# Kernel optimization log

Hardware: AMD Instinct MI355X
Metric: run time of the kernel (lower is better)

Reference implementation:

```python
import jax, jax.numpy as jnp
import numpy as np


def setup_inputs() -> dict:
    key = jax.random.key(0)
    ks = jax.random.split(key, 20)
    B, T, E, U, D, O = 64, 2048, 256, 256, 256, 32000
    s = lambda k, shp, fan: (jax.random.normal(k, shp, jnp.float32) * (1.0 / np.sqrt(fan)))
    return {
        'inputs': jax.random.normal(ks[0], (B, D), jnp.float32),
        'stm': jax.random.normal(ks[1], (B, U), jnp.float32),
        'x_seq': jax.random.normal(ks[2], (B, T, E), jnp.float32),
        'V_a': s(ks[3], (U + E,), U + E),
        'W_a': s(ks[4], (U + E, U + E), U + E),
        'W_r': s(ks[5], (D, U), D), 'U_r': s(ks[6], (U, U), U), 'C_r': s(ks[7], (E, U), E), 'b_r': jnp.zeros((U,), jnp.float32),
        'W_z': s(ks[8], (D, U), D), 'U_z': s(ks[9], (U, U), U), 'C_z': s(ks[10], (E, U), E), 'b_z': jnp.zeros((U,), jnp.float32),
        'W_p': s(ks[11], (D, U), D), 'U_p': s(ks[12], (U, U), U), 'C_p': s(ks[13], (E, U), E), 'b_p': jnp.zeros((U,), jnp.float32),
        'W_o': s(ks[14], (D, O), D), 'U_o': s(ks[15], (U, O), U), 'C_o': s(ks[16], (E, O), E), 'b_o': jnp.zeros((O,), jnp.float32),
    }


def reference(inputs, stm, x_seq, V_a, W_a,
              W_r, U_r, C_r, b_r,
              W_z, U_z, C_z, b_z,
              W_p, U_p, C_p, b_p,
              W_o, U_o, C_o, b_o):
    B, T, E = x_seq.shape
    U = stm.shape[-1]
    # Bahdanau additive attention: concat repeated state with encoder seq
    _stm = jnp.broadcast_to(stm[:, None, :], (B, T, U))          # [B,T,U]
    cat = jnp.concatenate([_stm, x_seq], axis=-1)                 # [B,T,U+E]
    et = jnp.einsum('btc,c->bt', jnp.tanh(jnp.einsum('btc,cd->btd', cat, W_a)), V_a)
    at = jax.nn.softmax(et, axis=1)                               # exp / sum over T
    context = jnp.einsum('bt,bte->be', at, x_seq)                 # [B,E]
    # GRU-style gates conditioned on input, previous state, and context
    rt = jax.nn.sigmoid(inputs @ W_r + stm @ U_r + context @ C_r + b_r)
    zt = jax.nn.sigmoid(inputs @ W_z + stm @ U_z + context @ C_z + b_z)
    s_tp = jnp.tanh(inputs @ W_p + (rt * stm) @ U_p + context @ C_p + b_p)
    st = (1.0 - zt) * stm + zt * s_tp                             # new state [B,U]
    output = jax.nn.softmax(inputs @ W_o + stm @ U_o + context @ C_o + b_o, axis=-1)  # [B,O]
    return output, st
```

## Files before the change

### kernel.cpp

```cpp
#include <hip/hip_runtime.h>
#include <hip/hip_bf16.h>

#define B_ 64
#define T_ 2048
#define E_ 256
#define U_ 256
#define O_ 32000
#define UE_ 512

typedef __attribute__((ext_vector_type(8))) short bf16x8;
typedef __attribute__((ext_vector_type(4))) float f32x4;

__device__ __forceinline__ unsigned short f2bf(float f){
  __hip_bfloat16 h = __float2bfloat16(f);
  return __builtin_bit_cast(unsigned short, h);
}
__device__ __forceinline__ unsigned pk2bf(float a, float b){
  return (unsigned)f2bf(a) | ((unsigned)f2bf(b) << 16);
}
__device__ __forceinline__ bf16x8 pack8(const float* v0, const float* v1){
  float4 x = *(const float4*)v0;
  float4 y = *(const float4*)v1;
  uint4 pk;
  pk.x = pk2bf(x.x, x.y); pk.y = pk2bf(x.z, x.w);
  pk.z = pk2bf(y.x, y.y); pk.w = pk2bf(y.z, y.w);
  return __builtin_bit_cast(bf16x8, pk);
}
__device__ __forceinline__ float ftanh(float x){
  float e = __expf(2.0f*x);
  return 1.0f - 2.0f/(e + 1.0f);
}
__device__ __forceinline__ float fsig(float x){
  return 1.0f/(1.0f + __expf(-x));
}

__global__ void pack_b_kernel(const float* __restrict__ Wa, unsigned short* __restrict__ bpack){
  int idx = blockIdx.x*256 + threadIdx.x;
  int n = idx & 511;
  int ktg = idx >> 9;
  int erow = ktg * 8;
  unsigned short o[8];
#pragma unroll
  for (int i = 0; i < 8; ++i)
    o[i] = f2bf(Wa[(256 + erow + i)*512 + n]);
  uint4 v;
  v.x = (unsigned)o[0] | ((unsigned)o[1] << 16);
  v.y = (unsigned)o[2] | ((unsigned)o[3] << 16);
  v.z = (unsigned)o[4] | ((unsigned)o[5] << 16);
  v.w = (unsigned)o[6] | ((unsigned)o[7] << 16);
  ((uint4*)bpack)[idx] = v;
}

__global__ __launch_bounds__(256)
void stmpart_mfma_kernel(const float* __restrict__ stm, const float* __restrict__ Wa,
                         float* __restrict__ sp){
  int tid = threadIdx.x;
  int w = tid >> 6, l = tid & 63, c = l & 15, g = l >> 4;
  int n0 = blockIdx.x*64 + w*16;
  f32x4 zero = {0.f,0.f,0.f,0.f};
  f32x4 acc[4];
#pragma unroll
  for (int mt = 0; mt < 4; ++mt) acc[mt] = zero;
#pragma unroll
  for (int ks = 0; ks < 8; ++ks){
    int kg = ks*32 + 8*g;
    bf16x8 a[4];
#pragma unroll
    for (int mt = 0; mt < 4; ++mt){
      const float* ap = stm + (mt*16 + c)*256 + kg;
      a[mt] = pack8(ap, ap + 4);
    }
    const float* bpt = Wa + (size_t)kg*512 + n0 + c;
    float bv[8];
#pragma unroll
    for (int i = 0; i < 8; ++i) bv[i] = bpt[(size_t)i*512];
    uint4 pk;
    pk.x = pk2bf(bv[0], bv[1]); pk.y = pk2bf(bv[2], bv[3]);
    pk.z = pk2bf(bv[4], bv[5]); pk.w = pk2bf(bv[6], bv[7]);
    bf16x8 bfr = __builtin_bit_cast(bf16x8, pk);
#pragma unroll
    for (int mt = 0; mt < 4; ++mt)
      acc[mt] = __builtin_amdgcn_mfma_f32_16x16x32_bf16(a[mt], bfr, acc[mt], 0, 0, 0);
  }
#pragma unroll
  for (int mt = 0; mt < 4; ++mt)
#pragma unroll
    for (int r = 0; r < 4; ++r){
      int m = mt*16 + 4*g + r;
      sp[m*512 + n0 + c] = acc[mt][r];
    }
}

__global__ __launch_bounds__(512, 4)
void et_kernel(const float* __restrict__ xseq, const unsigned short* __restrict__ bpack,
               const float* __restrict__ va, const float* __restrict__ sp,
               float* __restrict__ et){
  __shared__ __align__(16) uint4 sA4[2048];
  __shared__ float sVa[512];
  __shared__ float sSp[512];
  __shared__ float sEt[8][64];
  int tid = threadIdx.x;
  int m0 = blockIdx.x * 64;
  int b  = m0 >> 11;

  const float4* x4 = (const float4*)xseq + (size_t)m0 * 64;
  uint2* sA2 = (uint2*)sA4;
#pragma unroll
  for (int i = 0; i < 8; ++i){
    int p = i*512 + tid;
    int row = p >> 6, kq = p & 63;
    float4 v = x4[row*64 + kq];
    uint2 u;
    u.x = pk2bf(v.x, v.y);
    u.y = pk2bf(v.z, v.w);
    int s = ((row>>4)*8 + (kq>>3))*64 + ((kq>>1)&3)*16 + (row&15);
    sA2[(s ^ ((s>>4)&7))*2 + (kq&1)] = u;
  }
  sVa[tid < 512 ? tid : 0] = va[tid];
  sSp[tid] = sp[b*512 + tid];
  __syncthreads();

  int w = tid >> 6, l = tid & 63, c = l & 15, g = l >> 4;
  f32x4 zero = {0.f, 0.f, 0.f, 0.f};
  f32x4 acc[4][4];
#pragma unroll
  for (int mt = 0; mt < 4; ++mt)
#pragma unroll
    for (int nt = 0; nt < 4; ++nt) acc[mt][nt] = zero;

  const bf16x8* bp = (const bf16x8*)bpack;
#pragma unroll
  for (int ks = 0; ks < 8; ++ks){
    bf16x8 a[4], bb[4];
#pragma unroll
    for (int mt = 0; mt < 4; ++mt){
      int idx = (mt*8 + ks)*64 + l;
      a[mt] = *(const bf16x8*)&sA4[idx ^ ((idx>>4)&7)];
    }
    int bbase = (ks*4 + g)*512 + w*64 + c;
#pragma unroll
    for (int nt = 0; nt < 4; ++nt)
      bb[nt] = bp[bbase + nt*16];
#pragma unroll
    for (int mt = 0; mt < 4; ++mt)
#pragma unroll
      for (int nt = 0; nt < 4; ++nt)
        acc[mt][nt] = __builtin_amdgcn_mfma_f32_16x16x32_bf16(a[mt], bb[nt], acc[mt][nt], 0, 0, 0);
  }

  float pr[4][4];
#pragma unroll
  for (int mt = 0; mt < 4; ++mt)
#pragma unroll
    for (int r = 0; r < 4; ++r){
      float p = 0.f;
#pragma unroll
      for (int nt = 0; nt < 4; ++nt){
        int n = w*64 + nt*16 + c;
        float v = acc[mt][nt][r] + sSp[n];
        p += sVa[n] * ftanh(v);
      }
      pr[mt][r] = p;
    }
#pragma unroll
  for (int mask = 1; mask < 16; mask <<= 1){
#pragma unroll
    for (int mt = 0; mt < 4; ++mt)
#pragma unroll
      for (int r = 0; r < 4; ++r)
        pr[mt][r] += __shfl_xor(pr[mt][r], mask, 64);
  }
  if (c == 0){
#pragma unroll
    for (int mt = 0; mt < 4; ++mt)
#pragma unroll
      for (int r = 0; r < 4; ++r)
        sEt[w][mt*16 + 4*g + r] = pr[mt][r];
  }
  __syncthreads();
  if (tid < 64){
    float e = 0.f;
#pragma unroll
    for (int ww = 0; ww < 8; ++ww) e += sEt[ww][tid];
    et[m0 + tid] = e;
  }
}

__global__ void at_kernel(const float* __restrict__ et, float* __restrict__ at){
  __shared__ float red[4];
  __shared__ float red2[4];
  int b = blockIdx.x, tid = threadIdx.x;
  float v[8];
#pragma unroll
  for (int i = 0; i < 8; ++i) v[i] = et[b*2048 + i*256 + tid];
  float m = v[0];
#pragma unroll
  for (int i = 1; i < 8; ++i) m = fmaxf(m, v[i]);
#pragma unroll
  for (int off = 1; off < 64; off <<= 1) m = fmaxf(m, __shfl_xor(m, off, 64));
  int wv = tid >> 6;
  if ((tid & 63) == 0) red[wv] = m;
  __syncthreads();
  m = fmaxf(fmaxf(red[0], red[1]), fmaxf(red[2], red[3]));
  float e[8]; float s = 0.f;
#pragma unroll
  for (int i = 0; i < 8; ++i){ e[i] = __expf(v[i] - m); s += e[i]; }
#pragma unroll
  for (int off = 1; off < 64; off <<= 1) s += __shfl_xor(s, off, 64);
  if ((tid & 63) == 0) red2[wv] = s;
  __syncthreads();
  s = red2[0] + red2[1] + red2[2] + red2[3];
  float inv = 1.0f / s;
#pragma unroll
  for (int i = 0; i < 8; ++i) at[b*2048 + i*256 + tid] = e[i] * inv;
}

__global__ void ctxpart_kernel(const float* __restrict__ at, const float* __restrict__ xseq,
                               float* __restrict__ cp){
  __shared__ float s_at[256];
  int ch = blockIdx.x;
  int b  = blockIdx.y;
  int e  = threadIdx.x;
  int t0 = ch * 256;
  s_at[e] = at[b*2048 + t0 + e];
  __syncthreads();
  float acc = 0.f;
  const float* xp = xseq + ((size_t)(b*2048 + t0))*256 + e;
#pragma unroll 4
  for (int tt = 0; tt < 256; ++tt)
    acc += s_at[tt] * xp[(size_t)tt * 256];
  cp[(b*8 + ch)*256 + e] = acc;
}

__global__ void ctx_x1_kernel(const float* __restrict__ cp, const float* __restrict__ inputs,
                              const float* __restrict__ stm,
                              unsigned short* __restrict__ X1bf){
  int b = blockIdx.x, e = threadIdx.x;
  float s = 0.f;
#pragma unroll
  for (int c = 0; c < 8; ++c) s += cp[(b*8 + c)*256 + e];
  X1bf[b*768 + e]        = f2bf(inputs[b*256 + e]);
  X1bf[b*768 + 256 + e]  = f2bf(stm[b*256 + e]);
  X1bf[b*768 + 512 + e]  = f2bf(s);
}

__global__ __launch_bounds__(256)
void gates1_kernel(const unsigned short* __restrict__ X1bf, const float* __restrict__ stm,
                   const float* __restrict__ Wr, const float* __restrict__ Ur,
                   const float* __restrict__ Cr, const float* __restrict__ brr,
                   const float* __restrict__ Wz, const float* __restrict__ Uz,
                   const float* __restrict__ Cz, const float* __restrict__ bzz,
                   const float* __restrict__ Wp, const float* __restrict__ Cp,
                   const float* __restrict__ bpp,
                   float* __restrict__ rs, float* __restrict__ ztb, float* __restrict__ pic){
  int tid = threadIdx.x;
  int w = tid >> 6, l = tid & 63, c = l & 15, g = l >> 4;
  int n0 = blockIdx.x*64 + w*16;
  int gate = n0 >> 8;
  int col0 = n0 & 255;
  const float* W0; const float* W1; const float* W2; const float* bias;
  if (gate == 0){ W0 = Wr; W1 = Ur; W2 = Cr; bias = brr; }
  else if (gate == 1){ W0 = Wz; W1 = Uz; W2 = Cz; bias = bzz; }
  else { W0 = Wp; W1 = nullptr; W2 = Cp; bias = bpp; }

  f32x4 zero = {0.f,0.f,0.f,0.f};
  f32x4 acc[4];
#pragma unroll
  for (int mt = 0; mt < 4; ++mt) acc[mt] = zero;

#pragma unroll
  for (int ph = 0; ph < 3; ++ph){
    const float* src = (ph == 0) ? W0 : (ph == 1) ? W1 : W2;
    if (src == nullptr) continue;
#pragma unroll
    for (int ks = 0; ks < 8; ++ks){
      int kg = ks*32 + 8*g;
      bf16x8 a[4];
#pragma unroll
      for (int mt = 0; mt < 4; ++mt)
        a[mt] = *(const bf16x8*)&X1bf[(mt*16 + c)*768 + ph*256 + kg];
      const float* bpt = src + (size_t)kg*256 + col0 + c;
      float bv[8];
#pragma unroll
      for (int i = 0; i < 8; ++i) bv[i] = bpt[(size_t)i*256];
      uint4 pk;
      pk.x = pk2bf(bv[0], bv[1]); pk.y = pk2bf(bv[2], bv[3]);
      pk.z = pk2bf(bv[4], bv[5]); pk.w = pk2bf(bv[6], bv[7]);
      bf16x8 bfr = __builtin_bit_cast(bf16x8, pk);
#pragma unroll
      for (int mt = 0; mt < 4; ++mt)
        acc[mt] = __builtin_amdgcn_mfma_f32_16x16x32_bf16(a[mt], bfr, acc[mt], 0, 0, 0);
    }
  }

  int n = col0 + c;
  float bi = bias[n];
#pragma unroll
  for (int mt = 0; mt < 4; ++mt)
#pragma unroll
    for (int r = 0; r < 4; ++r){
      int m = mt*16 + 4*g + r;
      float pre = acc[mt][r] + bi;
      if (gate == 0)      rs[m*256 + n]  = fsig(pre) * stm[m*256 + n];
      else if (gate == 1) ztb[m*256 + n] = fsig(pre);
      else                pic[m*256 + n] = pre;
    }
}

__global__ __launch_bounds__(256)
void gates2_kernel(const float* __restrict__ rs, const float* __restrict__ Up,
                   const float* __restrict__ pic, const float* __restrict__ ztb,
                   const float* __restrict__ stm, float* __restrict__ stout){
  int tid = threadIdx.x;
  int w = tid >> 6, l = tid & 63, c = l & 15, g = l >> 4;
  int n0 = blockIdx.x*64 + w*16;
  f32x4 zero = {0.f,0.f,0.f,0.f};
  f32x4 acc[4];
#pragma unroll
  for (int mt = 0; mt < 4; ++mt) acc[mt] = zero;
#pragma unroll
  for (int ks = 0; ks < 8; ++ks){
    int kg = ks*32 + 8*g;
    bf16x8 a[4];
#pragma unroll
    for (int mt = 0; mt < 4; ++mt){
      const float* ap = rs + (mt*16 + c)*256 + kg;
      a[mt] = pack8(ap, ap + 4);
    }
    const float* bpt = Up + (size_t)kg*256 + n0 + c;
    float bv[8];
#pragma unroll
    for (int i = 0; i < 8; ++i) bv[i] = bpt[(size_t)i*256];
    uint4 pk;
    pk.x = pk2bf(bv[0], bv[1]); pk.y = pk2bf(bv[2], bv[3]);
    pk.z = pk2bf(bv[4], bv[5]); pk.w = pk2bf(bv[6], bv[7]);
    bf16x8 bfr = __builtin_bit_cast(bf16x8, pk);
#pragma unroll
    for (int mt = 0; mt < 4; ++mt)
      acc[mt] = __builtin_amdgcn_mfma_f32_16x16x32_bf16(a[mt], bfr, acc[mt], 0, 0, 0);
  }
#pragma unroll
  for (int mt = 0; mt < 4; ++mt)
#pragma unroll
    for (int r = 0; r < 4; ++r){
      int m = mt*16 + 4*g + r;
      int o = m*256 + n0 + c;
      float ap = pic[o] + acc[mt][r];
      float z = ztb[o];
      stout[o] = (1.f - z)*stm[o] + z*ftanh(ap);
    }
}

__global__ __launch_bounds__(256)
void logits_mfma_kernel(const unsigned short* __restrict__ X1bf,
                        const float* __restrict__ Wo, const float* __restrict__ Uo,
                        const float* __restrict__ Co, const float* __restrict__ boo,
                        float* __restrict__ outl){
  int tid = threadIdx.x;
  int w = tid >> 6, l = tid & 63, c = l & 15, g = l >> 4;
  int n0 = blockIdx.x*64 + w*16;
  f32x4 zero = {0.f,0.f,0.f,0.f};
  f32x4 acc[4];
#pragma unroll
  for (int mt = 0; mt < 4; ++mt) acc[mt] = zero;

#pragma unroll
  for (int ph = 0; ph < 3; ++ph){
    const float* src = (ph == 0) ? Wo : (ph == 1) ? Uo : Co;
#pragma unroll 2
    for (int ks = 0; ks < 8; ++ks){
      int kg = ph*256 + ks*32 + 8*g;
      bf16x8 a[4];
#pragma unroll
      for (int mt = 0; mt < 4; ++mt)
        a[mt] = *(const bf16x8*)&X1bf[(mt*16 + c)*768 + kg];
      const float* bpt = src + (size_t)(ks*32 + 8*g)*32000 + n0 + c;
      float bv[8];
#pragma unroll
      for (int i = 0; i < 8; ++i) bv[i] = bpt[(size_t)i*32000];
      uint4 pk;
      pk.x = pk2bf(bv[0], bv[1]);
      pk.y = pk2bf(bv[2], bv[3]);
      pk.z = pk2bf(bv[4], bv[5]);
      pk.w = pk2bf(bv[6], bv[7]);
      bf16x8 bfr = __builtin_bit_cast(bf16x8, pk);
#pragma unroll
      for (int mt = 0; mt < 4; ++mt)
        acc[mt] = __builtin_amdgcn_mfma_f32_16x16x32_bf16(a[mt], bfr, acc[mt], 0, 0, 0);
    }
  }

  float bias = boo[n0 + c];
#pragma unroll
  for (int mt = 0; mt < 4; ++mt)
#pragma unroll
    for (int r = 0; r < 4; ++r){
      int m = mt*16 + 4*g + r;
      outl[(size_t)m*32000 + n0 + c] = acc[mt][r] + bias;
    }
}

__global__ void sm_part_kernel(const float* __restrict__ logits, float* __restrict__ part){
  __shared__ float red[4];
  __shared__ float red2[4];
  int bid = blockIdx.x;
  int b = bid >> 3, ch = bid & 7;
  int base = b*32000 + ch*4000;
  int tid = threadIdx.x;
  float v[16];
#pragma unroll
  for (int i = 0; i < 16; ++i){
    int idx = i*256 + tid;
    v[i] = (idx < 4000) ? logits[base + idx] : -INFINITY;
  }
  float m = v[0];
#pragma unroll
  for (int i = 1; i < 16; ++i) m = fmaxf(m, v[i]);
#pragma unroll
  for (int off = 1; off < 64; off <<= 1) m = fmaxf(m, __shfl_xor(m, off, 64));
  int wv = tid >> 6;
  if ((tid & 63) == 0) red[wv] = m;
  __syncthreads();
  m = fmaxf(fmaxf(red[0], red[1]), fmaxf(red[2], red[3]));
  float s = 0.f;
#pragma unroll
  for (int i = 0; i < 16; ++i) s += __expf(v[i] - m);
#pragma unroll
  for (int off = 1; off < 64; off <<= 1) s += __shfl_xor(s, off, 64);
  if ((tid & 63) == 0) red2[wv] = s;
  __syncthreads();
  if (tid == 0){
    float st = red2[0] + red2[1] + red2[2] + red2[3];
    part[bid*2]     = m;
    part[bid*2 + 1] = st;
  }
}

__global__ void sm_norm_kernel(float* __restrict__ logits, const float* __restrict__ part){
  int bid = blockIdx.x;
  int b = bid >> 3, ch = bid & 7;
  int base = b*32000 + ch*4000;
  int tid = threadIdx.x;
  float M = -INFINITY;
#pragma unroll
  for (int cc = 0; cc < 8; ++cc) M = fmaxf(M, part[(b*8 + cc)*2]);
  float S = 0.f;
#pragma unroll
  for (int cc = 0; cc < 8; ++cc) S += part[(b*8 + cc)*2 + 1] * __expf(part[(b*8 + cc)*2] - M);
  float inv = 1.0f / S;
#pragma unroll
  for (int i = 0; i < 16; ++i){
    int idx = i*256 + tid;
    if (idx < 4000){
      int o = base + idx;
      logits[o] = __expf(logits[o] - M) * inv;
    }
  }
}

extern "C" void kernel_launch(void* const* d_in, const int* in_sizes, int n_in,
                              void* d_out, int out_size, void* d_ws, size_t ws_size,
                              hipStream_t stream) {
  const float* inputs = (const float*)d_in[0];
  const float* stm    = (const float*)d_in[1];
  const float* xseq   = (const float*)d_in[2];
  const float* Va     = (const float*)d_in[3];
  const float* Wa     = (const float*)d_in[4];
  const float* Wr = (const float*)d_in[5];
  const float* Ur = (const float*)d_in[6];
  const float* Cr = (const float*)d_in[7];
  const float* br = (const float*)d_in[8];
  const float* Wz = (const float*)d_in[9];
  const float* Uz = (const float*)d_in[10];
  const float* Cz = (const float*)d_in[11];
  const float* bz = (const float*)d_in[12];
  const float* Wp = (const float*)d_in[13];
  const float* Up = (const float*)d_in[14];
  const float* Cp = (const float*)d_in[15];
  const float* bp = (const float*)d_in[16];
  const float* Wo = (const float*)d_in[17];
  const float* Uo = (const float*)d_in[18];
  const float* Co = (const float*)d_in[19];
  const float* bo = (const float*)d_in[20];

  float* out   = (float*)d_out;
  float* stout = out + (size_t)B_*O_;

  float* wsf = (float*)d_ws;
  unsigned short* bpack = (unsigned short*)d_ws;
  float* sp   = wsf + 65536;
  float* et   = wsf + 98304;
  float* at   = wsf + 229376;
  float* cp   = wsf + 360448;
  unsigned short* X1bf = (unsigned short*)(wsf + 491520);
  float* part = wsf + 516096;
  float* rs   = wsf + 517120;
  float* ztb  = wsf + 533504;
  float* pic  = wsf + 549888;

  pack_b_kernel<<<64, 256, 0, stream>>>(Wa, bpack);
  stmpart_mfma_kernel<<<8, 256, 0, stream>>>(stm, Wa, sp);
  et_kernel<<<2048, 512, 0, stream>>>(xseq, bpack, Va, sp, et);
  at_kernel<<<64, 256, 0, stream>>>(et, at);
  ctxpart_kernel<<<dim3(8, 64), 256, 0, stream>>>(at, xseq, cp);
  ctx_x1_kernel<<<64, 256, 0, stream>>>(cp, inputs, stm, X1bf);
  gates1_kernel<<<12, 256, 0, stream>>>(X1bf, stm, Wr, Ur, Cr, br,
                                        Wz, Uz, Cz, bz, Wp, Cp, bp,
                                        rs, ztb, pic);
  gates2_kernel<<<4, 256, 0, stream>>>(rs, Up, pic, ztb, stm, stout);
  logits_mfma_kernel<<<500, 256, 0, stream>>>(X1bf, Wo, Uo, Co, bo, out);
  sm_part_kernel<<<512, 256, 0, stream>>>(out, part);
  sm_norm_kernel<<<512, 256, 0, stream>>>(out, part);
}
```

Measured before the change: 175.2 us.

## Fuse softmax partial stats into logits GEMM and preload et B-fragments into registers

The logits GEMM epilogue now computes per-block row max and exp-sum and writes them as partials, so the softmax no longer re-reads the full 64x32000 logits just to gather statistics. A small combine kernel merges the 500 partials per row, and the normalize pass uses the final stats. Separately, et_kernel loads all its B fragments into registers before staging A, which lets the global loads overlap the LDS fill; the occupancy hint in launch bounds is dropped, which raises register pressure.

After: 198.9 us. 13.5% more time.

```diff
diff --git a/kernel.cpp b/kernel.cpp
--- a/kernel.cpp
+++ b/kernel.cpp
@@ -91,7 +91,7 @@
     }
 }
 
-__global__ __launch_bounds__(512, 4)
+__global__ __launch_bounds__(512)
 void et_kernel(const float* __restrict__ xseq, const unsigned short* __restrict__ bpack,
                const float* __restrict__ va, const float* __restrict__ sp,
                float* __restrict__ et){
@@ -100,8 +100,19 @@
   __shared__ float sSp[512];
   __shared__ float sEt[8][64];
   int tid = threadIdx.x;
+  int w = tid >> 6, l = tid & 63, c = l & 15, g = l >> 4;
   int m0 = blockIdx.x * 64;
   int b  = m0 >> 11;
+
+  const bf16x8* bp = (const bf16x8*)bpack;
+  bf16x8 breg[8][4];
+#pragma unroll
+  for (int ks = 0; ks < 8; ++ks){
+    int bbase = (ks*4 + g)*512 + w*64 + c;
+#pragma unroll
+    for (int nt = 0; nt < 4; ++nt)
+      breg[ks][nt] = bp[bbase + nt*16];
+  }
 
   const float4* x4 = (const float4*)xseq + (size_t)m0 * 64;
   uint2* sA2 = (uint2*)sA4;
@@ -116,11 +127,10 @@
     int s = ((row>>4)*8 + (kq>>3))*64 + ((kq>>1)&3)*16 + (row&15);
     sA2[(s ^ ((s>>4)&7))*2 + (kq&1)] = u;
   }
-  sVa[tid < 512 ? tid : 0] = va[tid];
+  sVa[tid] = va[tid];
   sSp[tid] = sp[b*512 + tid];
   __syncthreads();
 
-  int w = tid >> 6, l = tid & 63, c = l & 15, g = l >> 4;
   f32x4 zero = {0.f, 0.f, 0.f, 0.f};
   f32x4 acc[4][4];
 #pragma unroll
@@ -128,24 +138,19 @@
 #pragma unroll
     for (int nt = 0; nt < 4; ++nt) acc[mt][nt] = zero;
 
-  const bf16x8* bp = (const bf16x8*)bpack;
 #pragma unroll
   for (int ks = 0; ks < 8; ++ks){
-    bf16x8 a[4], bb[4];
+    bf16x8 a[4];
 #pragma unroll
     for (int mt = 0; mt < 4; ++mt){
       int idx = (mt*8 + ks)*64 + l;
       a[mt] = *(const bf16x8*)&sA4[idx ^ ((idx>>4)&7)];
     }
-    int bbase = (ks*4 + g)*512 + w*64 + c;
-#pragma unroll
-    for (int nt = 0; nt < 4; ++nt)
-      bb[nt] = bp[bbase + nt*16];
 #pragma unroll
     for (int mt = 0; mt < 4; ++mt)
 #pragma unroll
       for (int nt = 0; nt < 4; ++nt)
-        acc[mt][nt] = __builtin_amdgcn_mfma_f32_16x16x32_bf16(a[mt], bb[nt], acc[mt][nt], 0, 0, 0);
+        acc[mt][nt] = __builtin_amdgcn_mfma_f32_16x16x32_bf16(a[mt], breg[ks][nt], acc[mt][nt], 0, 0, 0);
   }
 
   float pr[4][4];
@@ -355,7 +360,7 @@
 void logits_mfma_kernel(const unsigned short* __restrict__ X1bf,
                         const float* __restrict__ Wo, const float* __restrict__ Uo,
                         const float* __restrict__ Co, const float* __restrict__ boo,
-                        float* __restrict__ outl){
+                        float* __restrict__ outl, float* __restrict__ part){
   int tid = threadIdx.x;
   int w = tid >> 6, l = tid & 63, c = l & 15, g = l >> 4;
   int n0 = blockIdx.x*64 + w*16;
@@ -391,63 +396,109 @@
   }
 
   float bias = boo[n0 + c];
+  float v[4][4];
 #pragma unroll
   for (int mt = 0; mt < 4; ++mt)
 #pragma unroll
     for (int r = 0; r < 4; ++r){
       int m = mt*16 + 4*g + r;
-      outl[(size_t)m*32000 + n0 + c] = acc[mt][r] + bias;
-    }
-}
-
-__global__ void sm_part_kernel(const float* __restrict__ logits, float* __restrict__ part){
-  __shared__ float red[4];
-  __shared__ float red2[4];
+      v[mt][r] = acc[mt][r] + bias;
+      outl[(size_t)m*32000 + n0 + c] = v[mt][r];
+    }
+
+  __shared__ float sMx[4][64];
+  __shared__ float sSx[4][64];
+  float mx[4][4];
+#pragma unroll
+  for (int mt = 0; mt < 4; ++mt)
+#pragma unroll
+    for (int r = 0; r < 4; ++r) mx[mt][r] = v[mt][r];
+#pragma unroll
+  for (int mask = 1; mask < 16; mask <<= 1)
+#pragma unroll
+    for (int mt = 0; mt < 4; ++mt)
+#pragma unroll
+      for (int r = 0; r < 4; ++r)
+        mx[mt][r] = fmaxf(mx[mt][r], __shfl_xor(mx[mt][r], mask, 64));
+  if (c == 0)
+#pragma unroll
+    for (int mt = 0; mt < 4; ++mt)
+#pragma unroll
+      for (int r = 0; r < 4; ++r)
+        sMx[w][mt*16 + 4*g + r] = mx[mt][r];
+  __syncthreads();
+  float sx[4][4];
+#pragma unroll
+  for (int mt = 0; mt < 4; ++mt)
+#pragma unroll
+    for (int r = 0; r < 4; ++r){
+      int row = mt*16 + 4*g + r;
+      float M = fmaxf(fmaxf(sMx[0][row], sMx[1][row]), fmaxf(sMx[2][row], sMx[3][row]));
+      sx[mt][r] = __expf(v[mt][r] - M);
+    }
+#pragma unroll
+  for (int mask = 1; mask < 16; mask <<= 1)
+#pragma unroll
+    for (int mt = 0; mt < 4; ++mt)
+#pragma unroll
+      for (int r = 0; r < 4; ++r)
+        sx[mt][r] += __shfl_xor(sx[mt][r], mask, 64);
+  if (c == 0)
+#pragma unroll
+    for (int mt = 0; mt < 4; ++mt)
+#pragma unroll
+      for (int r = 0; r < 4; ++r)
+        sSx[w][mt*16 + 4*g + r] = sx[mt][r];
+  __syncthreads();
+  if (tid < 64){
+    int row = tid;
+    float M = fmaxf(fmaxf(sMx[0][row], sMx[1][row]), fmaxf(sMx[2][row], sMx[3][row]));
+    float S = sSx[0][row] + sSx[1][row] + sSx[2][row] + sSx[3][row];
+    part[blockIdx.x*128 + row*2]     = M;
+    part[blockIdx.x*128 + row*2 + 1] = S;
+  }
+}
+
+__global__ void sm_comb_kernel(const float* __restrict__ part, float* __restrict__ fin){
+  __shared__ float red[8];
+  __shared__ float red2[8];
+  int b = blockIdx.x;
+  int tid = threadIdx.x;
+  float M = -INFINITY, S = 0.f;
+  if (tid < 500){
+    M = part[tid*128 + b*2];
+    S = part[tid*128 + b*2 + 1];
+  }
+  float m1 = M;
+#pragma unroll
+  for (int off = 1; off < 64; off <<= 1) m1 = fmaxf(m1, __shfl_xor(m1, off, 64));
+  int wv = tid >> 6;
+  if ((tid & 63) == 0) red[wv] = m1;
+  __syncthreads();
+  float Mg = red[0];
+#pragma unroll
+  for (int i = 1; i < 8; ++i) Mg = fmaxf(Mg, red[i]);
+  float s1 = (tid < 500) ? S * __expf(M - Mg) : 0.f;
+#pragma unroll
+  for (int off = 1; off < 64; off <<= 1) s1 += __shfl_xor(s1, off, 64);
+  if ((tid & 63) == 0) red2[wv] = s1;
+  __syncthreads();
+  if (tid == 0){
+    float St = 0.f;
+#pragma unroll
+    for (int i = 0; i < 8; ++i) St += red2[i];
+    fin[b*2] = Mg;
+    fin[b*2 + 1] = St;
+  }
+}
+
+__global__ void sm_norm_kernel(float* __restrict__ logits, const float* __restrict__ fin){
   int bid = blockIdx.x;
   int b = bid >> 3, ch = bid & 7;
   int base = b*32000 + ch*4000;
   int tid = threadIdx.x;
-  float v[16];
-#pragma unroll
-  for (int i = 0; i < 16; ++i){
-    int idx = i*256 + tid;
-    v[i] = (idx < 4000) ? logits[base + idx] : -INFINITY;
-  }
-  float m = v[0];
-#pragma unroll
-  for (int i = 1; i < 16; ++i) m = fmaxf(m, v[i]);
-#pragma unroll
-  for (int off = 1; off < 64; off <<= 1) m = fmaxf(m, __shfl_xor(m, off, 64));
-  int wv = tid >> 6;
-  if ((tid & 63) == 0) red[wv] = m;
-  __syncthreads();
-  m = fmaxf(fmaxf(red[0], red[1]), fmaxf(red[2], red[3]));
-  float s = 0.f;
-#pragma unroll
-  for (int i = 0; i < 16; ++i) s += __expf(v[i] - m);
-#pragma unroll
-  for (int off = 1; off < 64; off <<= 1) s += __shfl_xor(s, off, 64);
-  if ((tid & 63) == 0) red2[wv] = s;
-  __syncthreads();
-  if (tid == 0){
-    float st = red2[0] + red2[1] + red2[2] + red2[3];
-    part[bid*2]     = m;
-    part[bid*2 + 1] = st;
-  }
-}
-
-__global__ void sm_norm_kernel(float* __restrict__ logits, const float* __restrict__ part){
-  int bid = blockIdx.x;
-  int b = bid >> 3, ch = bid & 7;
-  int base = b*32000 + ch*4000;
-  int tid = threadIdx.x;
-  float M = -INFINITY;
-#pragma unroll
-  for (int cc = 0; cc < 8; ++cc) M = fmaxf(M, part[(b*8 + cc)*2]);
-  float S = 0.f;
-#pragma unroll
-  for (int cc = 0; cc < 8; ++cc) S += part[(b*8 + cc)*2 + 1] * __expf(part[(b*8 + cc)*2] - M);
-  float inv = 1.0f / S;
+  float M = fin[2*b];
+  float inv = 1.0f / fin[2*b + 1];
 #pragma unroll
   for (int i = 0; i < 16; ++i){
     int idx = i*256 + tid;
@@ -494,9 +545,10 @@
   float* cp   = wsf + 360448;
   unsigned short* X1bf = (unsigned short*)(wsf + 491520);
   float* part = wsf + 516096;
-  float* rs   = wsf + 517120;
-  float* ztb  = wsf + 533504;
-  float* pic  = wsf + 549888;
+  float* fin  = wsf + 580096;
+  float* rs   = wsf + 580224;
+  float* ztb  = wsf + 596608;
+  float* pic  = wsf + 612992;
 
   pack_b_kernel<<<64, 256, 0, stream>>>(Wa, bpack);
   stmpart_mfma_kernel<<<8, 256, 0, stream>>>(stm, Wa, sp);
@@ -508,7 +560,7 @@
                                         Wz, Uz, Cz, bz, Wp, Cp, bp,
                                         rs, ztb, pic);
   gates2_kernel<<<4, 256, 0, stream>>>(rs, Up, pic, ztb, stm, stout);
-  logits_mfma_kernel<<<500, 256, 0, stream>>>(X1bf, Wo, Uo, Co, bo, out);
-  sm_part_kernel<<<512, 256, 0, stream>>>(out, part);
-  sm_norm_kernel<<<512, 256, 0, stream>>>(out, part);
-}
+  logits_mfma_kernel<<<500, 256, 0, stream>>>(X1bf, Wo, Uo, Co, bo, out, part);
+  sm_comb_kernel<<<64, 512, 0, stream>>>(part, fin);
+  sm_norm_kernel<<<512, 256, 0, stream>>>(out, fin);
+}
```

## Merge prep kernels, transpose et MFMA operands, split-K logits across two wave groups

Applied to the files above, without the earlier changes.

Fuses the bpack packing and the stm projection into one launch to cut one kernel launch. In et_kernel it swaps the MFMA operand roles so that W_a is the A operand and the x tile is the B operand. The per-row tanh·V_a reduction then needs two cross-lane shuffles instead of four and reads V_a and sp as float4. The logits kernel doubles its block to 512 threads and splits the K loop between two wave groups, combining the partial sums through shared memory to add memory-level parallelism on the 32000-wide weight stream, at the cost of a barrier and extra LDS.

Measured after the change: 177.1 us. About the same (+1.1%).

```diff
diff --git a/kernel.cpp b/kernel.cpp
--- a/kernel.cpp
+++ b/kernel.cpp
@@ -34,61 +34,61 @@
   return 1.0f/(1.0f + __expf(-x));
 }
 
-__global__ void pack_b_kernel(const float* __restrict__ Wa, unsigned short* __restrict__ bpack){
-  int idx = blockIdx.x*256 + threadIdx.x;
-  int n = idx & 511;
-  int ktg = idx >> 9;
-  int erow = ktg * 8;
-  unsigned short o[8];
-#pragma unroll
-  for (int i = 0; i < 8; ++i)
-    o[i] = f2bf(Wa[(256 + erow + i)*512 + n]);
-  uint4 v;
-  v.x = (unsigned)o[0] | ((unsigned)o[1] << 16);
-  v.y = (unsigned)o[2] | ((unsigned)o[3] << 16);
-  v.z = (unsigned)o[4] | ((unsigned)o[5] << 16);
-  v.w = (unsigned)o[6] | ((unsigned)o[7] << 16);
-  ((uint4*)bpack)[idx] = v;
-}
-
 __global__ __launch_bounds__(256)
-void stmpart_mfma_kernel(const float* __restrict__ stm, const float* __restrict__ Wa,
-                         float* __restrict__ sp){
-  int tid = threadIdx.x;
-  int w = tid >> 6, l = tid & 63, c = l & 15, g = l >> 4;
-  int n0 = blockIdx.x*64 + w*16;
-  f32x4 zero = {0.f,0.f,0.f,0.f};
-  f32x4 acc[4];
-#pragma unroll
-  for (int mt = 0; mt < 4; ++mt) acc[mt] = zero;
-#pragma unroll
-  for (int ks = 0; ks < 8; ++ks){
-    int kg = ks*32 + 8*g;
-    bf16x8 a[4];
-#pragma unroll
-    for (int mt = 0; mt < 4; ++mt){
-      const float* ap = stm + (mt*16 + c)*256 + kg;
-      a[mt] = pack8(ap, ap + 4);
-    }
-    const float* bpt = Wa + (size_t)kg*512 + n0 + c;
-    float bv[8];
-#pragma unroll
-    for (int i = 0; i < 8; ++i) bv[i] = bpt[(size_t)i*512];
-    uint4 pk;
-    pk.x = pk2bf(bv[0], bv[1]); pk.y = pk2bf(bv[2], bv[3]);
-    pk.z = pk2bf(bv[4], bv[5]); pk.w = pk2bf(bv[6], bv[7]);
-    bf16x8 bfr = __builtin_bit_cast(bf16x8, pk);
+void prep_kernel(const float* __restrict__ Wa, const float* __restrict__ stm,
+                 unsigned short* __restrict__ bpack, float* __restrict__ sp){
+  if (blockIdx.x < 64){
+    int idx = blockIdx.x*256 + threadIdx.x;
+    int n = idx & 511;
+    int ktg = idx >> 9;
+    int erow = ktg * 8;
+    unsigned short o[8];
+#pragma unroll
+    for (int i = 0; i < 8; ++i)
+      o[i] = f2bf(Wa[(256 + erow + i)*512 + n]);
+    uint4 v;
+    v.x = (unsigned)o[0] | ((unsigned)o[1] << 16);
+    v.y = (unsigned)o[2] | ((unsigned)o[3] << 16);
+    v.z = (unsigned)o[4] | ((unsigned)o[5] << 16);
+    v.w = (unsigned)o[6] | ((unsigned)o[7] << 16);
+    ((uint4*)bpack)[idx] = v;
+  } else {
+    int tid = threadIdx.x;
+    int w = tid >> 6, l = tid & 63, c = l & 15, g = l >> 4;
+    int n0 = (blockIdx.x - 64)*64 + w*16;
+    f32x4 zero = {0.f,0.f,0.f,0.f};
+    f32x4 acc[4];
+#pragma unroll
+    for (int mt = 0; mt < 4; ++mt) acc[mt] = zero;
+#pragma unroll
+    for (int ks = 0; ks < 8; ++ks){
+      int kg = ks*32 + 8*g;
+      bf16x8 a[4];
+#pragma unroll
+      for (int mt = 0; mt < 4; ++mt){
+        const float* ap = stm + (mt*16 + c)*256 + kg;
+        a[mt] = pack8(ap, ap + 4);
+      }
+      const float* bpt = Wa + (size_t)kg*512 + n0 + c;
+      float bv[8];
+#pragma unroll
+      for (int i = 0; i < 8; ++i) bv[i] = bpt[(size_t)i*512];
+      uint4 pk;
+      pk.x = pk2bf(bv[0], bv[1]); pk.y = pk2bf(bv[2], bv[3]);
+      pk.z = pk2bf(bv[4], bv[5]); pk.w = pk2bf(bv[6], bv[7]);
+      bf16x8 bfr = __builtin_bit_cast(bf16x8, pk);
+#pragma unroll
+      for (int mt = 0; mt < 4; ++mt)
+        acc[mt] = __builtin_amdgcn_mfma_f32_16x16x32_bf16(a[mt], bfr, acc[mt], 0, 0, 0);
+    }
 #pragma unroll
     for (int mt = 0; mt < 4; ++mt)
-      acc[mt] = __builtin_amdgcn_mfma_f32_16x16x32_bf16(a[mt], bfr, acc[mt], 0, 0, 0);
-  }
-#pragma unroll
-  for (int mt = 0; mt < 4; ++mt)
-#pragma unroll
-    for (int r = 0; r < 4; ++r){
-      int m = mt*16 + 4*g + r;
-      sp[m*512 + n0 + c] = acc[mt][r];
-    }
+#pragma unroll
+      for (int r = 0; r < 4; ++r){
+        int m = mt*16 + 4*g + r;
+        sp[m*512 + n0 + c] = acc[mt][r];
+      }
+  }
 }
 
 __global__ __launch_bounds__(512, 4)
@@ -100,6 +100,7 @@
   __shared__ float sSp[512];
   __shared__ float sEt[8][64];
   int tid = threadIdx.x;
+  int w = tid >> 6, l = tid & 63, c = l & 15, g = l >> 4;
   int m0 = blockIdx.x * 64;
   int b  = m0 >> 11;
 
@@ -116,66 +117,61 @@
     int s = ((row>>4)*8 + (kq>>3))*64 + ((kq>>1)&3)*16 + (row&15);
     sA2[(s ^ ((s>>4)&7))*2 + (kq&1)] = u;
   }
-  sVa[tid < 512 ? tid : 0] = va[tid];
+  sVa[tid] = va[tid];
   sSp[tid] = sp[b*512 + tid];
   __syncthreads();
 
-  int w = tid >> 6, l = tid & 63, c = l & 15, g = l >> 4;
   f32x4 zero = {0.f, 0.f, 0.f, 0.f};
   f32x4 acc[4][4];
 #pragma unroll
   for (int mt = 0; mt < 4; ++mt)
 #pragma unroll
-    for (int nt = 0; nt < 4; ++nt) acc[mt][nt] = zero;
+    for (int tc = 0; tc < 4; ++tc) acc[mt][tc] = zero;
 
   const bf16x8* bp = (const bf16x8*)bpack;
 #pragma unroll
   for (int ks = 0; ks < 8; ++ks){
-    bf16x8 a[4], bb[4];
-#pragma unroll
-    for (int mt = 0; mt < 4; ++mt){
-      int idx = (mt*8 + ks)*64 + l;
-      a[mt] = *(const bf16x8*)&sA4[idx ^ ((idx>>4)&7)];
-    }
+    bf16x8 aw[4], bx[4];
     int bbase = (ks*4 + g)*512 + w*64 + c;
 #pragma unroll
-    for (int nt = 0; nt < 4; ++nt)
-      bb[nt] = bp[bbase + nt*16];
-#pragma unroll
     for (int mt = 0; mt < 4; ++mt)
-#pragma unroll
-      for (int nt = 0; nt < 4; ++nt)
-        acc[mt][nt] = __builtin_amdgcn_mfma_f32_16x16x32_bf16(a[mt], bb[nt], acc[mt][nt], 0, 0, 0);
-  }
-
-  float pr[4][4];
-#pragma unroll
-  for (int mt = 0; mt < 4; ++mt)
-#pragma unroll
-    for (int r = 0; r < 4; ++r){
-      float p = 0.f;
-#pragma unroll
-      for (int nt = 0; nt < 4; ++nt){
-        int n = w*64 + nt*16 + c;
-        float v = acc[mt][nt][r] + sSp[n];
-        p += sVa[n] * ftanh(v);
+      aw[mt] = bp[bbase + mt*16];
+#pragma unroll
+    for (int tc = 0; tc < 4; ++tc){
+      int idx = (tc*8 + ks)*64 + l;
+      bx[tc] = *(const bf16x8*)&sA4[idx ^ ((idx>>4)&7)];
+    }
+#pragma unroll
+    for (int mt = 0; mt < 4; ++mt)
+#pragma unroll
+      for (int tc = 0; tc < 4; ++tc)
+        acc[mt][tc] = __builtin_amdgcn_mfma_f32_16x16x32_bf16(aw[mt], bx[tc], acc[mt][tc], 0, 0, 0);
+  }
+
+  float p[4] = {0.f, 0.f, 0.f, 0.f};
+#pragma unroll
+  for (int mt = 0; mt < 4; ++mt){
+    int nb = w*64 + mt*16 + 4*g;
+    float4 vav = *(const float4*)&sVa[nb];
+    float4 spv = *(const float4*)&sSp[nb];
+#pragma unroll
+    for (int tc = 0; tc < 4; ++tc){
+#pragma unroll
+      for (int r = 0; r < 4; ++r){
+        float vv = acc[mt][tc][r] + ((const float*)&spv)[r];
+        p[tc] += ((const float*)&vav)[r] * ftanh(vv);
       }
-      pr[mt][r] = p;
-    }
-#pragma unroll
-  for (int mask = 1; mask < 16; mask <<= 1){
-#pragma unroll
-    for (int mt = 0; mt < 4; ++mt)
-#pragma unroll
-      for (int r = 0; r < 4; ++r)
-        pr[mt][r] += __shfl_xor(pr[mt][r], mask, 64);
-  }
-  if (c == 0){
-#pragma unroll
-    for (int mt = 0; mt < 4; ++mt)
-#pragma unroll
-      for (int r = 0; r < 4; ++r)
-        sEt[w][mt*16 + 4*g + r] = pr[mt][r];
+    }
+  }
+#pragma unroll
+  for (int tc = 0; tc < 4; ++tc){
+    p[tc] += __shfl_xor(p[tc], 16, 64);
+    p[tc] += __shfl_xor(p[tc], 32, 64);
+  }
+  if (l < 16){
+#pragma unroll
+    for (int tc = 0; tc < 4; ++tc)
+      sEt[w][tc*16 + c] = p[tc];
   }
   __syncthreads();
   if (tid < 64){
@@ -351,14 +347,17 @@
     }
 }
 
-__global__ __launch_bounds__(256)
+__global__ __launch_bounds__(512)
 void logits_mfma_kernel(const unsigned short* __restrict__ X1bf,
                         const float* __restrict__ Wo, const float* __restrict__ Uo,
                         const float* __restrict__ Co, const float* __restrict__ boo,
                         float* __restrict__ outl){
+  __shared__ float sAcc[16][4][64];
   int tid = threadIdx.x;
   int w = tid >> 6, l = tid & 63, c = l & 15, g = l >> 4;
-  int n0 = blockIdx.x*64 + w*16;
+  int wc = w & 3;
+  int kh = w >> 2;
+  int n0 = blockIdx.x*64 + wc*16;
   f32x4 zero = {0.f,0.f,0.f,0.f};
   f32x4 acc[4];
 #pragma unroll
@@ -367,8 +366,9 @@
 #pragma unroll
   for (int ph = 0; ph < 3; ++ph){
     const float* src = (ph == 0) ? Wo : (ph == 1) ? Uo : Co;
-#pragma unroll 2
-    for (int ks = 0; ks < 8; ++ks){
+#pragma unroll
+    for (int kss = 0; kss < 4; ++kss){
+      int ks = 2*kss + kh;
       int kg = ph*256 + ks*32 + 8*g;
       bf16x8 a[4];
 #pragma unroll
@@ -390,14 +390,25 @@
     }
   }
 
-  float bias = boo[n0 + c];
-#pragma unroll
-  for (int mt = 0; mt < 4; ++mt)
-#pragma unroll
-    for (int r = 0; r < 4; ++r){
-      int m = mt*16 + 4*g + r;
-      outl[(size_t)m*32000 + n0 + c] = acc[mt][r] + bias;
-    }
+  if (kh == 1){
+#pragma unroll
+    for (int mt = 0; mt < 4; ++mt)
+#pragma unroll
+      for (int r = 0; r < 4; ++r)
+        sAcc[mt*4 + r][wc][l] = acc[mt][r];
+  }
+  __syncthreads();
+  if (kh == 0){
+    float bias = boo[n0 + c];
+#pragma unroll
+    for (int mt = 0; mt < 4; ++mt)
+#pragma unroll
+      for (int r = 0; r < 4; ++r){
+        int m = mt*16 + 4*g + r;
+        float vv = acc[mt][r] + sAcc[mt*4 + r][wc][l] + bias;
+        outl[(size_t)m*32000 + n0 + c] = vv;
+      }
+  }
 }
 
 __global__ void sm_part_kernel(const float* __restrict__ logits, float* __restrict__ part){
@@ -498,8 +509,7 @@
   float* ztb  = wsf + 533504;
   float* pic  = wsf + 549888;
 
-  pack_b_kernel<<<64, 256, 0, stream>>>(Wa, bpack);
-  stmpart_mfma_kernel<<<8, 256, 0, stream>>>(stm, Wa, sp);
+  prep_kernel<<<72, 256, 0, stream>>>(Wa, stm, bpack, sp);
   et_kernel<<<2048, 512, 0, stream>>>(xseq, bpack, Va, sp, et);
   at_kernel<<<64, 256, 0, stream>>>(et, at);
   ctxpart_kernel<<<dim3(8, 64), 256, 0, stream>>>(at, xseq, cp);
@@ -508,7 +518,7 @@
                                         Wz, Uz, Cz, bz, Wp, Cp, bp,
                                         rs, ztb, pic);
   gates2_kernel<<<4, 256, 0, stream>>>(rs, Up, pic, ztb, stm, stout);
-  logits_mfma_kernel<<<500, 256, 0, stream>>>(X1bf, Wo, Uo, Co, bo, out);
+  logits_mfma_kernel<<<500, 512, 0, stream>>>(X1bf, Wo, Uo, Co, bo, out);
   sm_part_kernel<<<512, 256, 0, stream>>>(out, part);
   sm_norm_kernel<<<512, 256, 0, stream>>>(out, part);
 }
```
